# Kernel tuning notes

Hardware: AMD Instinct MI355X
Metric: run time of the kernel (lower is better)

The kernel has to match this reference:

```python
import jax, jax.numpy as jnp
import numpy as np

N_USER = 80000
N_ITEM = 20000
N = N_USER + N_ITEM          # total nodes
E = 1600000                  # edges (nnz of norm_adj), avg degree 16
EMB = 64                     # emb_size
FEAT = 64                    # feature_dim -> input_dim = 128
D = EMB + FEAT               # 128
L = 3                        # number of GCN layers, layer_size=[128,128,128]
K = 3                        # max_hop
B = 4096                     # batch_size


def setup_inputs() -> dict:
    key = jax.random.key(0)
    ks = jax.random.split(key, 16)
    deg_scale = 1.0 / 16.0  # ~normalized adjacency values
    return {
        'edge_row': jax.random.randint(ks[0], (E,), 0, N, dtype=jnp.int32),
        'edge_col': jax.random.randint(ks[1], (E,), 0, N, dtype=jnp.int32),
        'edge_val': jax.random.uniform(ks[2], (E,), dtype=jnp.float32) * deg_scale,
        'feat': jax.random.normal(ks[3], (N_USER, FEAT), dtype=jnp.float32) * 0.1,
        'user_emb': jax.random.normal(ks[4], (N_USER, EMB), dtype=jnp.float32) * 0.1,
        'item_emb1': jax.random.normal(ks[5], (N_ITEM, EMB), dtype=jnp.float32) * 0.1,
        'item_emb2': jax.random.normal(ks[6], (N_ITEM, FEAT), dtype=jnp.float32) * 0.1,
        'alphas': jax.random.normal(ks[7], (L, K), dtype=jnp.float32) * 0.1,
        'W_gc': jax.random.normal(ks[8], (L, D, D), dtype=jnp.float32) * 0.05,
        'b_gc': jax.random.normal(ks[9], (L, 1, D), dtype=jnp.float32) * 0.05,
        'W_bi': jax.random.normal(ks[10], (L, D, D), dtype=jnp.float32) * 0.05,
        'b_bi': jax.random.normal(ks[11], (L, 1, D), dtype=jnp.float32) * 0.05,
        'users': jax.random.randint(ks[12], (B,), 0, N_USER, dtype=jnp.int32),
        'pos_items': jax.random.randint(ks[13], (B,), 0, N_ITEM, dtype=jnp.int32),
        'neg_items': jax.random.randint(ks[14], (B,), 0, N_ITEM, dtype=jnp.int32),
    }


def reference(edge_row, edge_col, edge_val, feat, user_emb, item_emb1,
              item_emb2, alphas, W_gc, b_gc, W_bi, b_bi,
              users, pos_items, neg_items):
    def spmm(X):
        # A_hat @ X via edge-list gather + segment-sum (sparse.mm equivalent)
        return jax.ops.segment_sum(edge_val[:, None] * X[edge_col], edge_row,
                                   num_segments=N)

    # ego embeddings: [[user_emb|feat], [item_emb1|item_emb2]] -> [N, D]
    ego = jnp.concatenate([
        jnp.concatenate([user_emb, item_emb1], axis=0),
        jnp.concatenate([feat, item_emb2], axis=0),
    ], axis=1)

    all_embs = [ego]
    for k in range(L):
        # multi-order aggregation: sum_i beta_i * A^i @ ego
        beta = jax.nn.softmax(alphas[k])
        cur = spmm(ego)
        side = beta[0] * cur
        for i in range(1, K):
            cur = spmm(cur)
            side = side + beta[i] * cur
        sum_e = side @ W_gc[k] + b_gc[k]
        bi_e = (ego * side) @ W_bi[k] + b_bi[k]
        # aggregator_mode == 'sum_bi'
        ego = jax.nn.leaky_relu(sum_e, negative_slope=0.2) + bi_e
        # mess_dropout = 0 -> identity; L2-normalize rows (F.normalize eps=1e-12)
        norm = ego / jnp.maximum(
            jnp.linalg.norm(ego, axis=1, keepdims=True), 1e-12)
        all_embs.append(norm)

    all_emb = jnp.concatenate(all_embs, axis=1)  # [N, D*(L+1)] = [N, 512]
    u_emb = all_emb[:N_USER]
    i_emb = all_emb[N_USER:]
    return (u_emb[users], i_emb[pos_items], i_emb[neg_items])
```

## Files before the change

### kernel.cpp

```cpp
#include <hip/hip_runtime.h>
#include <hip/hip_bf16.h>

typedef __hip_bfloat16 hbf16;
typedef unsigned short u16;
typedef __bf16 bf16x8 __attribute__((ext_vector_type(8)));
typedef float f32x4 __attribute__((ext_vector_type(4)));

#define N_USERS 80000
#define N_ITEMS 20000
#define NTOT    100000
#define NEDGE   1600000
#define DDIM    128
#define NLAY    3
#define KHOP    3
#define NB      4096
#define SCAN_BS 1024
#define LBM     128

__device__ inline u16 f2bfu(float f) { __bf16 h = (__bf16)f; return __builtin_bit_cast(u16, h); }

__global__ void beta_kernel(const float* __restrict__ alphas, float* __restrict__ beta) {
    if (threadIdx.x == 0 && blockIdx.x == 0) {
        for (int k = 0; k < NLAY; ++k) {
            float a[KHOP];
            float m = -1e30f;
            for (int i = 0; i < KHOP; ++i) { a[i] = alphas[k*KHOP+i]; m = fmaxf(m, a[i]); }
            float s = 0.f;
            for (int i = 0; i < KHOP; ++i) { a[i] = expf(a[i] - m); s += a[i]; }
            for (int i = 0; i < KHOP; ++i) beta[k*KHOP+i] = a[i] / s;
        }
    }
}

__global__ void build_ego_kernel(const float* __restrict__ feat, const float* __restrict__ user_emb,
                                 const float* __restrict__ item_emb1, const float* __restrict__ item_emb2,
                                 u16* __restrict__ ego) {
    int i = blockIdx.x * 256 + threadIdx.x;
    int n = i >> 7, d = i & 127;
    float v;
    if (n < N_USERS) {
        v = (d < 64) ? user_emb[n*64 + d] : feat[n*64 + d - 64];
    } else {
        int m = n - N_USERS;
        v = (d < 64) ? item_emb1[m*64 + d] : item_emb2[m*64 + d - 64];
    }
    ego[i] = f2bfu(v);
}

__global__ void transpose_w_kernel(const float* __restrict__ Wgc, const float* __restrict__ Wbi,
                                   u16* __restrict__ WTgc, u16* __restrict__ WTbi) {
    __shared__ float t[32][33];
    int z = blockIdx.z;
    const float* W = (z < 3) ? (Wgc + (size_t)z * 16384) : (Wbi + (size_t)(z - 3) * 16384);
    u16* WT = (z < 3) ? (WTgc + (size_t)z * 16384) : (WTbi + (size_t)(z - 3) * 16384);
    int r0 = blockIdx.y * 32, c0 = blockIdx.x * 32;
    for (int i = threadIdx.y; i < 32; i += 8)
        t[i][threadIdx.x] = W[(size_t)(r0 + i) * 128 + c0 + threadIdx.x];
    __syncthreads();
    for (int i = threadIdx.y; i < 32; i += 8)
        WT[(size_t)(c0 + i) * 128 + r0 + threadIdx.x] = f2bfu(t[threadIdx.x][i]);
}

__global__ void zero_kernel(int* __restrict__ p, int n) {
    int i = blockIdx.x * 256 + threadIdx.x;
    if (i < n) p[i] = 0;
}

__global__ void hist_kernel(const int* __restrict__ er, int* __restrict__ counts) {
    int i = blockIdx.x * 256 + threadIdx.x;
    if (i < NEDGE) atomicAdd(&counts[er[i]], 1);
}

__global__ void scan1_kernel(const int* __restrict__ counts, int* __restrict__ rowptr,
                             int* __restrict__ bsums, int n) {
    __shared__ int sm[SCAN_BS];
    int i = blockIdx.x * SCAN_BS + threadIdx.x;
    int v = (i < n) ? counts[i] : 0;
    sm[threadIdx.x] = v;
    __syncthreads();
    for (int off = 1; off < SCAN_BS; off <<= 1) {
        int t = (threadIdx.x >= off) ? sm[threadIdx.x - off] : 0;
        __syncthreads();
        sm[threadIdx.x] += t;
        __syncthreads();
    }
    if (i < n) rowptr[i] = sm[threadIdx.x] - v;
    if (threadIdx.x == SCAN_BS - 1) bsums[blockIdx.x] = sm[SCAN_BS - 1];
}

__global__ void scan2_kernel(int* __restrict__ bsums, int nb) {
    if (threadIdx.x == 0 && blockIdx.x == 0) {
        int acc = 0;
        for (int b = 0; b < nb; ++b) { int t = bsums[b]; bsums[b] = acc; acc += t; }
    }
}

__global__ void scan3_kernel(int* __restrict__ rowptr, const int* __restrict__ bsums,
                             int* __restrict__ counters, int n) {
    int i = blockIdx.x * SCAN_BS + threadIdx.x;
    if (i < n) {
        int v = rowptr[i] + bsums[blockIdx.x];
        rowptr[i] = v;
        counters[i] = v;
    }
    if (blockIdx.x == 0 && threadIdx.x == 0) rowptr[n] = NEDGE;
}

__global__ void scatter_kernel(const int* __restrict__ er, const int* __restrict__ ec,
                               const float* __restrict__ ev, int* __restrict__ counters,
                               int2* __restrict__ edges) {
    int i = blockIdx.x * 256 + threadIdx.x;
    if (i < NEDGE) {
        int r = er[i];
        int p = atomicAdd(&counters[r], 1);
        unsigned long long rec = ((unsigned long long)(unsigned)__float_as_int(ev[i]) << 32)
                               | (unsigned)ec[i];
        __builtin_nontemporal_store(rec, reinterpret_cast<unsigned long long*>(edges + p));
    }
}

__global__ __launch_bounds__(256) void spmm_kernel(
    const int* __restrict__ rowptr, const int2* __restrict__ edges,
    const u16* __restrict__ X, u16* __restrict__ Y) {
    int tid = threadIdx.x;
    int r = blockIdx.x * 16 + (tid >> 4);
    int lane = tid & 15;
    int s = rowptr[r], e = rowptr[r + 1];
    float acc[8];
    #pragma unroll
    for (int i = 0; i < 8; ++i) acc[i] = 0.f;
    const u16* xb = X + lane * 8;
    int j = s;
    for (; j + 4 <= e; j += 4) {
        int2 e0 = edges[j+0], e1 = edges[j+1], e2 = edges[j+2], e3 = edges[j+3];
        bf16x8 x0 = *reinterpret_cast<const bf16x8*>(xb + (size_t)e0.x * DDIM);
        bf16x8 x1 = *reinterpret_cast<const bf16x8*>(xb + (size_t)e1.x * DDIM);
        bf16x8 x2 = *reinterpret_cast<const bf16x8*>(xb + (size_t)e2.x * DDIM);
        bf16x8 x3 = *reinterpret_cast<const bf16x8*>(xb + (size_t)e3.x * DDIM);
        float v0 = __int_as_float(e0.y), v1 = __int_as_float(e1.y);
        float v2 = __int_as_float(e2.y), v3 = __int_as_float(e3.y);
        #pragma unroll
        for (int i = 0; i < 8; ++i) acc[i] = fmaf(v0, (float)x0[i], acc[i]);
        #pragma unroll
        for (int i = 0; i < 8; ++i) acc[i] = fmaf(v1, (float)x1[i], acc[i]);
        #pragma unroll
        for (int i = 0; i < 8; ++i) acc[i] = fmaf(v2, (float)x2[i], acc[i]);
        #pragma unroll
        for (int i = 0; i < 8; ++i) acc[i] = fmaf(v3, (float)x3[i], acc[i]);
    }
    for (; j < e; ++j) {
        int2 ed = edges[j];
        float v = __int_as_float(ed.y);
        bf16x8 x = *reinterpret_cast<const bf16x8*>(xb + (size_t)ed.x * DDIM);
        #pragma unroll
        for (int i = 0; i < 8; ++i) acc[i] = fmaf(v, (float)x[i], acc[i]);
    }
    size_t oi = (size_t)r * DDIM + lane * 8;
    bf16x8 y;
    #pragma unroll
    for (int i = 0; i < 8; ++i) y[i] = (__bf16)acc[i];
    *reinterpret_cast<bf16x8*>(Y + oi) = y;
}

__global__ __launch_bounds__(512) void layer_kernel(
    const u16* __restrict__ ego, const u16* __restrict__ h1,
    const u16* __restrict__ h2, const u16* __restrict__ h3,
    const float* __restrict__ beta3,
    const u16* __restrict__ wtgc, const u16* __restrict__ wtbi,
    const float* __restrict__ bgc, const float* __restrict__ bbi,
    u16* __restrict__ ego_out, u16* __restrict__ normbuf) {
    __shared__ __align__(16) unsigned char smem[131072];
    const int AS = 0, AB = 32768, WG = 65536, WB = 98304;
    int tid = threadIdx.x;
    int base = blockIdx.x * LBM;
    float b0 = beta3[0], b1 = beta3[1], b2 = beta3[2];

    {
        int row = tid >> 2, q = tid & 3;
        int grow = base + row;
        bool ok = grow < NTOT;
        size_t roff = (size_t)grow * DDIM + q * 32;
        int sw = (row & 7) << 4;
        #pragma unroll
        for (int cg = 0; cg < 4; ++cg) {
            bf16x8 pa, pb;
            if (ok) {
                bf16x8 x1 = *reinterpret_cast<const bf16x8*>(h1 + roff + cg * 8);
                bf16x8 x2 = *reinterpret_cast<const bf16x8*>(h2 + roff + cg * 8);
                bf16x8 x3 = *reinterpret_cast<const bf16x8*>(h3 + roff + cg * 8);
                bf16x8 ev = *reinterpret_cast<const bf16x8*>(ego + roff + cg * 8);
                #pragma unroll
                for (int i = 0; i < 8; ++i) {
                    float sf = b0 * (float)x1[i] + b1 * (float)x2[i] + b2 * (float)x3[i];
                    pa[i] = (__bf16)sf;
                    pb[i] = (__bf16)(sf * (float)ev[i]);
                }
            } else {
                #pragma unroll
                for (int i = 0; i < 8; ++i) { pa[i] = (__bf16)0.f; pb[i] = (__bf16)0.f; }
            }
            int kb = q * 64 + cg * 16;
            *reinterpret_cast<bf16x8*>(&smem[AS + row * 256 + (kb ^ sw)]) = pa;
            *reinterpret_cast<bf16x8*>(&smem[AB + row * 256 + (kb ^ sw)]) = pb;
        }
    }
    #pragma unroll
    for (int p = 0; p < 4; ++p) {
        int slot = tid + p * 512;
        int n = slot >> 4, ks = slot & 15;
        uint4 g  = *reinterpret_cast<const uint4*>(wtgc + n * DDIM + ks * 8);
        uint4 bq = *reinterpret_cast<const uint4*>(wtbi + n * DDIM + ks * 8);
        int addr = n * 256 + ((ks * 16) ^ ((n & 7) << 4));
        *reinterpret_cast<uint4*>(&smem[WG + addr]) = g;
        *reinterpret_cast<uint4*>(&smem[WB + addr]) = bq;
    }
    __syncthreads();

    int l = tid & 63, w = tid >> 6;
    int m = l & 15, g16 = l >> 4;
    int sw = (m & 7) << 4;
    int arow = (w * 16 + m) * 256;
    f32x4 accg[8], accb[8];
    #pragma unroll
    for (int nt = 0; nt < 8; ++nt) {
        accg[nt] = (f32x4){0.f, 0.f, 0.f, 0.f};
        accb[nt] = (f32x4){0.f, 0.f, 0.f, 0.f};
    }
    #pragma unroll
    for (int kk = 0; kk < 4; ++kk) {
        int ka = (kk * 64 + g16 * 16) ^ sw;
        bf16x8 as = *reinterpret_cast<const bf16x8*>(&smem[AS + arow + ka]);
        bf16x8 ab = *reinterpret_cast<const bf16x8*>(&smem[AB + arow + ka]);
        #pragma unroll
        for (int nt = 0; nt < 8; ++nt) {
            int na = (nt * 16 + m) * 256 + ka;
            bf16x8 bg = *reinterpret_cast<const bf16x8*>(&smem[WG + na]);
            accg[nt] = __builtin_amdgcn_mfma_f32_16x16x32_bf16(as, bg, accg[nt], 0, 0, 0);
            bf16x8 bb = *reinterpret_cast<const bf16x8*>(&smem[WB + na]);
            accb[nt] = __builtin_amdgcn_mfma_f32_16x16x32_bf16(ab, bb, accb[nt], 0, 0, 0);
        }
    }
    float bgv[8], bbv[8];
    #pragma unroll
    for (int nt = 0; nt < 8; ++nt) { bgv[nt] = bgc[nt * 16 + m]; bbv[nt] = bbi[nt * 16 + m]; }
    float vv[8][4];
    float ss[4] = {0.f, 0.f, 0.f, 0.f};
    #pragma unroll
    for (int nt = 0; nt < 8; ++nt) {
        #pragma unroll
        for (int rr = 0; rr < 4; ++rr) {
            float se = accg[nt][rr] + bgv[nt];
            float be = accb[nt][rr] + bbv[nt];
            float v = (se > 0.f ? se : 0.2f * se) + be;
            vv[nt][rr] = v;
            ss[rr] += v * v;
            int row = base + w * 16 + g16 * 4 + rr;
            if (row < NTOT) ego_out[(size_t)row * DDIM + nt * 16 + m] = f2bfu(v);
        }
    }
    #pragma unroll
    for (int rr = 0; rr < 4; ++rr) {
        ss[rr] += __shfl_xor(ss[rr], 1, 64);
        ss[rr] += __shfl_xor(ss[rr], 2, 64);
        ss[rr] += __shfl_xor(ss[rr], 4, 64);
        ss[rr] += __shfl_xor(ss[rr], 8, 64);
        ss[rr] = 1.f / fmaxf(sqrtf(ss[rr]), 1e-12f);
    }
    #pragma unroll
    for (int nt = 0; nt < 8; ++nt) {
        #pragma unroll
        for (int rr = 0; rr < 4; ++rr) {
            int row = base + w * 16 + g16 * 4 + rr;
            if (row < NTOT) normbuf[(size_t)row * DDIM + nt * 16 + m] = f2bfu(vv[nt][rr] * ss[rr]);
        }
    }
}

__global__ void gather_ego_kernel(const float* __restrict__ feat, const float* __restrict__ user_emb,
                                  const float* __restrict__ item_emb1, const float* __restrict__ item_emb2,
                                  const int* __restrict__ users, const int* __restrict__ pos,
                                  const int* __restrict__ neg, float* __restrict__ out) {
    int i = blockIdx.x * 256 + threadIdx.x;
    int which = i / (NB * DDIM);
    int rem = i - which * (NB * DDIM);
    int b = rem >> 7, d = rem & 127;
    float v;
    if (which == 0) {
        int u = users[b];
        v = (d < 64) ? user_emb[u*64 + d] : feat[u*64 + d - 64];
    } else {
        int m = (which == 1) ? pos[b] : neg[b];
        v = (d < 64) ? item_emb1[m*64 + d] : item_emb2[m*64 + d - 64];
    }
    out[(size_t)which * NB * 512 + (size_t)b * 512 + d] = v;
}

__global__ void gather_slice_kernel(const u16* __restrict__ src, const int* __restrict__ users,
                                    const int* __restrict__ pos, const int* __restrict__ neg,
                                    float* __restrict__ out, int slot) {
    int i = blockIdx.x * 256 + threadIdx.x;
    int which = i / (NB * DDIM);
    int rem = i - which * (NB * DDIM);
    int b = rem >> 7, c = rem & 127;
    int row;
    if (which == 0)      row = users[b];
    else if (which == 1) row = N_USERS + pos[b];
    else                 row = N_USERS + neg[b];
    unsigned int u = src[(size_t)row * DDIM + c];
    out[(size_t)which * NB * 512 + (size_t)b * 512 + slot * 128 + c] =
        __builtin_bit_cast(float, u << 16);
}

extern "C" void kernel_launch(void* const* d_in, const int* in_sizes, int n_in,
                              void* d_out, int out_size, void* d_ws, size_t ws_size,
                              hipStream_t stream) {
    (void)in_sizes; (void)n_in; (void)out_size; (void)ws_size;
    const int*   edge_row  = (const int*)  d_in[0];
    const int*   edge_col  = (const int*)  d_in[1];
    const float* edge_val  = (const float*)d_in[2];
    const float* feat      = (const float*)d_in[3];
    const float* user_emb  = (const float*)d_in[4];
    const float* item_emb1 = (const float*)d_in[5];
    const float* item_emb2 = (const float*)d_in[6];
    const float* alphas    = (const float*)d_in[7];
    const float* W_gc      = (const float*)d_in[8];
    const float* b_gc      = (const float*)d_in[9];
    const float* W_bi      = (const float*)d_in[10];
    const float* b_bi      = (const float*)d_in[11];
    const int*   users     = (const int*)  d_in[12];
    const int*   pos_items = (const int*)  d_in[13];
    const int*   neg_items = (const int*)  d_in[14];
    float* out = (float*)d_out;

    char* ws = (char*)d_ws;
    size_t off = 0;
    auto alloc = [&](size_t bytes) -> char* {
        char* p = ws + off;
        off = (off + bytes + 255) & ~(size_t)255;
        return p;
    };
    u16*   ego      = (u16*)  alloc((size_t)NTOT * DDIM * 2);
    u16*   h1       = (u16*)  alloc((size_t)NTOT * DDIM * 2);
    u16*   h2       = (u16*)  alloc((size_t)NTOT * DDIM * 2);
    u16*   h3       = (u16*)  alloc((size_t)NTOT * DDIM * 2);
    u16*   normbuf  = (u16*)  alloc((size_t)NTOT * DDIM * 2);
    int*   rowptr   = (int*)  alloc((size_t)(NTOT + 1) * 4);
    int*   counts   = (int*)  alloc((size_t)NTOT * 4);
    int*   counters = (int*)  alloc((size_t)NTOT * 4);
    int*   bsums    = (int*)  alloc(4096);
    int2*  edges    = (int2*) alloc((size_t)NEDGE * 8);
    u16*   wtgc     = (u16*)  alloc((size_t)NLAY * DDIM * DDIM * 2);
    u16*   wtbi     = (u16*)  alloc((size_t)NLAY * DDIM * DDIM * 2);
    float* beta     = (float*)alloc(256);

    beta_kernel<<<1, 64, 0, stream>>>(alphas, beta);
    build_ego_kernel<<<(NTOT * DDIM) / 256, 256, 0, stream>>>(feat, user_emb, item_emb1, item_emb2, ego);
    transpose_w_kernel<<<dim3(4, 4, 6), dim3(32, 8), 0, stream>>>(W_gc, W_bi, wtgc, wtbi);

    zero_kernel<<<(NTOT + 255) / 256, 256, 0, stream>>>(counts, NTOT);
    hist_kernel<<<NEDGE / 256, 256, 0, stream>>>(edge_row, counts);
    int nblk = (NTOT + SCAN_BS - 1) / SCAN_BS;
    scan1_kernel<<<nblk, SCAN_BS, 0, stream>>>(counts, rowptr, bsums, NTOT);
    scan2_kernel<<<1, 64, 0, stream>>>(bsums, nblk);
    scan3_kernel<<<nblk, SCAN_BS, 0, stream>>>(rowptr, bsums, counters, NTOT);
    scatter_kernel<<<NEDGE / 256, 256, 0, stream>>>(edge_row, edge_col, edge_val, counters, edges);

    gather_ego_kernel<<<(3 * NB * DDIM) / 256, 256, 0, stream>>>(feat, user_emb, item_emb1, item_emb2,
                                                                 users, pos_items, neg_items, out);

    int lgrid = (NTOT + LBM - 1) / LBM;
    for (int k = 0; k < NLAY; ++k) {
        spmm_kernel<<<NTOT / 16, 256, 0, stream>>>(rowptr, edges, ego, h1);
        spmm_kernel<<<NTOT / 16, 256, 0, stream>>>(rowptr, edges, h1, h2);
        spmm_kernel<<<NTOT / 16, 256, 0, stream>>>(rowptr, edges, h2, h3);
        layer_kernel<<<lgrid, 512, 0, stream>>>(ego, h1, h2, h3, beta + 3 * k,
                                                wtgc + (size_t)k * DDIM * DDIM, wtbi + (size_t)k * DDIM * DDIM,
                                                b_gc + (size_t)k * DDIM, b_bi + (size_t)k * DDIM,
                                                ego, normbuf);
        gather_slice_kernel<<<(3 * NB * DDIM) / 256, 256, 0, stream>>>(normbuf, users, pos_items, neg_items, out, k + 1);
    }
}
```

Before: 937.2 us.

## Bucket edges by row range before CSR scatter; nontemporal edge loads in SpMM

```diff
diff --git a/kernel.cpp b/kernel.cpp
--- a/kernel.cpp
+++ b/kernel.cpp
@@ -16,6 +16,7 @@
 #define NB      4096
 #define SCAN_BS 1024
 #define LBM     128
+#define NBUK    49
 
 __device__ inline u16 f2bfu(float f) { __bf16 h = (__bf16)f; return __builtin_bit_cast(u16, h); }
 
@@ -66,9 +67,21 @@
     if (i < n) p[i] = 0;
 }
 
-__global__ void hist_kernel(const int* __restrict__ er, int* __restrict__ counts) {
-    int i = blockIdx.x * 256 + threadIdx.x;
-    if (i < NEDGE) atomicAdd(&counts[er[i]], 1);
+__global__ void hist_kernel(const int* __restrict__ er, int* __restrict__ counts,
+                            int* __restrict__ bbins) {
+    __shared__ int l[NBUK];
+    int tid = threadIdx.x;
+    for (int b = tid; b < NBUK; b += 256) l[b] = 0;
+    __syncthreads();
+    int i = blockIdx.x * 256 + tid;
+    if (i < NEDGE) {
+        int r = er[i];
+        atomicAdd(&counts[r], 1);
+        atomicAdd(&l[r >> 11], 1);
+    }
+    __syncthreads();
+    for (int b = tid; b < NBUK; b += 256)
+        if (l[b]) atomicAdd(&bbins[b], l[b]);
 }
 
 __global__ void scan1_kernel(const int* __restrict__ counts, int* __restrict__ rowptr,
@@ -106,17 +119,68 @@
     if (blockIdx.x == 0 && threadIdx.x == 0) rowptr[n] = NEDGE;
 }
 
-__global__ void scatter_kernel(const int* __restrict__ er, const int* __restrict__ ec,
-                               const float* __restrict__ ev, int* __restrict__ counters,
-                               int2* __restrict__ edges) {
-    int i = blockIdx.x * 256 + threadIdx.x;
-    if (i < NEDGE) {
-        int r = er[i];
-        int p = atomicAdd(&counters[r], 1);
-        unsigned long long rec = ((unsigned long long)(unsigned)__float_as_int(ev[i]) << 32)
-                               | (unsigned)ec[i];
-        __builtin_nontemporal_store(rec, reinterpret_cast<unsigned long long*>(edges + p));
-    }
+__global__ void bscan_kernel(const int* __restrict__ bbins, int* __restrict__ bbase,
+                             int* __restrict__ bcur) {
+    if (threadIdx.x == 0 && blockIdx.x == 0) {
+        int acc = 0;
+        for (int b = 0; b < NBUK; ++b) { int t = bbins[b]; bbase[b] = acc; bcur[b] = acc; acc += t; }
+        bbase[NBUK] = acc;
+    }
+}
+
+__global__ __launch_bounds__(256) void bappend_kernel(
+    const int* __restrict__ er, const int* __restrict__ ec, const float* __restrict__ ev,
+    int* __restrict__ bcur, int* __restrict__ tmprow, int2* __restrict__ tmpcv) {
+    __shared__ int lcnt[NBUK], lbase[NBUK], lrank[NBUK];
+    int tid = threadIdx.x;
+    for (int b = tid; b < NBUK; b += 256) { lcnt[b] = 0; lrank[b] = 0; }
+    __syncthreads();
+    int base = blockIdx.x * 2048;
+    int r[8], c[8], vb[8], bk[8];
+    bool ok[8];
+    #pragma unroll
+    for (int k = 0; k < 8; ++k) {
+        int i = base + k * 256 + tid;
+        ok[k] = i < NEDGE;
+        bk[k] = 0;
+        if (ok[k]) {
+            r[k] = er[i]; c[k] = ec[i]; vb[k] = __float_as_int(ev[i]);
+            bk[k] = r[k] >> 11;
+            atomicAdd(&lcnt[bk[k]], 1);
+        }
+    }
+    __syncthreads();
+    for (int b = tid; b < NBUK; b += 256)
+        lbase[b] = lcnt[b] ? atomicAdd(&bcur[b], lcnt[b]) : 0;
+    __syncthreads();
+    #pragma unroll
+    for (int k = 0; k < 8; ++k) {
+        if (ok[k]) {
+            int rank = atomicAdd(&lrank[bk[k]], 1);
+            int pos = lbase[bk[k]] + rank;
+            tmprow[pos] = r[k];
+            tmpcv[pos] = make_int2(c[k], vb[k]);
+        }
+    }
+}
+
+__global__ __launch_bounds__(1024) void bfinal_kernel(
+    const int* __restrict__ bbase, const int* __restrict__ tmprow,
+    const int2* __restrict__ tmpcv, int* __restrict__ counters, int2* __restrict__ edges) {
+    int b = blockIdx.x;
+    int s = bbase[b], e = bbase[b + 1];
+    for (int i = s + threadIdx.x; i < e; i += 1024) {
+        int row = tmprow[i];
+        int p = atomicAdd(&counters[row], 1);
+        edges[p] = tmpcv[i];
+    }
+}
+
+__device__ inline void ld_edge_nt(const int2* __restrict__ p, int& c, float& v) {
+    unsigned long long rec =
+        __builtin_nontemporal_load(reinterpret_cast<const unsigned long long*>(p));
+    c = (int)(unsigned)(rec & 0xffffffffull);
+    v = __int_as_float((int)(unsigned)(rec >> 32));
 }
 
 __global__ __launch_bounds__(256) void spmm_kernel(
@@ -131,29 +195,43 @@
     for (int i = 0; i < 8; ++i) acc[i] = 0.f;
     const u16* xb = X + lane * 8;
     int j = s;
+    for (; j + 8 <= e; j += 8) {
+        int cc[8]; float vv[8];
+        #pragma unroll
+        for (int u = 0; u < 8; ++u) ld_edge_nt(edges + j + u, cc[u], vv[u]);
+        bf16x8 x[8];
+        #pragma unroll
+        for (int u = 0; u < 8; ++u)
+            x[u] = *reinterpret_cast<const bf16x8*>(xb + (size_t)cc[u] * DDIM);
+        #pragma unroll
+        for (int u = 0; u < 8; ++u) {
+            #pragma unroll
+            for (int i = 0; i < 8; ++i) acc[i] = fmaf(vv[u], (float)x[u][i], acc[i]);
+        }
+    }
     for (; j + 4 <= e; j += 4) {
-        int2 e0 = edges[j+0], e1 = edges[j+1], e2 = edges[j+2], e3 = edges[j+3];
-        bf16x8 x0 = *reinterpret_cast<const bf16x8*>(xb + (size_t)e0.x * DDIM);
-        bf16x8 x1 = *reinterpret_cast<const bf16x8*>(xb + (size_t)e1.x * DDIM);
-        bf16x8 x2 = *reinterpret_cast<const bf16x8*>(xb + (size_t)e2.x * DDIM);
-        bf16x8 x3 = *reinterpret_cast<const bf16x8*>(xb + (size_t)e3.x * DDIM);
-        float v0 = __int_as_float(e0.y), v1 = __int_as_float(e1.y);
-        float v2 = __int_as_float(e2.y), v3 = __int_as_float(e3.y);
-        #pragma unroll
-        for (int i = 0; i < 8; ++i) acc[i] = fmaf(v0, (float)x0[i], acc[i]);
-        #pragma unroll
-        for (int i = 0; i < 8; ++i) acc[i] = fmaf(v1, (float)x1[i], acc[i]);
-        #pragma unroll
-        for (int i = 0; i < 8; ++i) acc[i] = fmaf(v2, (float)x2[i], acc[i]);
-        #pragma unroll
-        for (int i = 0; i < 8; ++i) acc[i] = fmaf(v3, (float)x3[i], acc[i]);
+        int cc[4]; float vv[4];
+        #pragma unroll
+        for (int u = 0; u < 4; ++u) ld_edge_nt(edges + j + u, cc[u], vv[u]);
+        bf16x8 x0 = *reinterpret_cast<const bf16x8*>(xb + (size_t)cc[0] * DDIM);
+        bf16x8 x1 = *reinterpret_cast<const bf16x8*>(xb + (size_t)cc[1] * DDIM);
+        bf16x8 x2 = *reinterpret_cast<const bf16x8*>(xb + (size_t)cc[2] * DDIM);
+        bf16x8 x3 = *reinterpret_cast<const bf16x8*>(xb + (size_t)cc[3] * DDIM);
+        #pragma unroll
+        for (int i = 0; i < 8; ++i) acc[i] = fmaf(vv[0], (float)x0[i], acc[i]);
+        #pragma unroll
+        for (int i = 0; i < 8; ++i) acc[i] = fmaf(vv[1], (float)x1[i], acc[i]);
+        #pragma unroll
+        for (int i = 0; i < 8; ++i) acc[i] = fmaf(vv[2], (float)x2[i], acc[i]);
+        #pragma unroll
+        for (int i = 0; i < 8; ++i) acc[i] = fmaf(vv[3], (float)x3[i], acc[i]);
     }
     for (; j < e; ++j) {
-        int2 ed = edges[j];
-        float v = __int_as_float(ed.y);
-        bf16x8 x = *reinterpret_cast<const bf16x8*>(xb + (size_t)ed.x * DDIM);
-        #pragma unroll
-        for (int i = 0; i < 8; ++i) acc[i] = fmaf(v, (float)x[i], acc[i]);
+        int cc; float vv;
+        ld_edge_nt(edges + j, cc, vv);
+        bf16x8 x = *reinterpret_cast<const bf16x8*>(xb + (size_t)cc * DDIM);
+        #pragma unroll
+        for (int i = 0; i < 8; ++i) acc[i] = fmaf(vv, (float)x[i], acc[i]);
     }
     size_t oi = (size_t)r * DDIM + lane * 8;
     bf16x8 y;
@@ -348,22 +426,32 @@
     int*   counts   = (int*)  alloc((size_t)NTOT * 4);
     int*   counters = (int*)  alloc((size_t)NTOT * 4);
     int*   bsums    = (int*)  alloc(4096);
+    int*   bbins    = (int*)  alloc((NBUK + 2) * 4);
+    int*   bbase    = (int*)  alloc((NBUK + 2) * 4);
+    int*   bcur     = (int*)  alloc((NBUK + 2) * 4);
     int2*  edges    = (int2*) alloc((size_t)NEDGE * 8);
     u16*   wtgc     = (u16*)  alloc((size_t)NLAY * DDIM * DDIM * 2);
     u16*   wtbi     = (u16*)  alloc((size_t)NLAY * DDIM * DDIM * 2);
     float* beta     = (float*)alloc(256);
 
+    int*  tmprow = (int*)h1;
+    int2* tmpcv  = (int2*)((char*)h1 + (size_t)NEDGE * 4);
+
     beta_kernel<<<1, 64, 0, stream>>>(alphas, beta);
     build_ego_kernel<<<(NTOT * DDIM) / 256, 256, 0, stream>>>(feat, user_emb, item_emb1, item_emb2, ego);
     transpose_w_kernel<<<dim3(4, 4, 6), dim3(32, 8), 0, stream>>>(W_gc, W_bi, wtgc, wtbi);
 
     zero_kernel<<<(NTOT + 255) / 256, 256, 0, stream>>>(counts, NTOT);
-    hist_kernel<<<NEDGE / 256, 256, 0, stream>>>(edge_row, counts);
+    zero_kernel<<<1, 64, 0, stream>>>(bbins, NBUK);
+    hist_kernel<<<(NEDGE + 255) / 256, 256, 0, stream>>>(edge_row, counts, bbins);
     int nblk = (NTOT + SCAN_BS - 1) / SCAN_BS;
     scan1_kernel<<<nblk, SCAN_BS, 0, stream>>>(counts, rowptr, bsums, NTOT);
     scan2_kernel<<<1, 64, 0, stream>>>(bsums, nblk);
     scan3_kernel<<<nblk, SCAN_BS, 0, stream>>>(rowptr, bsums, counters, NTOT);
-    scatter_kernel<<<NEDGE / 256, 256, 0, stream>>>(edge_row, edge_col, edge_val, counters, edges);
+    bscan_kernel<<<1, 64, 0, stream>>>(bbins, bbase, bcur);
+    bappend_kernel<<<(NEDGE + 2047) / 2048, 256, 0, stream>>>(edge_row, edge_col, edge_val,
+                                                              bcur, tmprow, tmpcv);
+    bfinal_kernel<<<NBUK, 1024, 0, stream>>>(bbase, tmprow, tmpcv, counters, edges);
 
     gather_ego_kernel<<<(3 * NB * DDIM) / 256, 256, 0, stream>>>(feat, user_emb, item_emb1, item_emb2,
                                                                  users, pos_items, neg_items, out);
```

Result: slower. 1.095 ms (+16.9%).
